# Optimization experiments

Hardware: AMD Instinct MI355X
Metric: run time of the kernel (lower is better)

The kernel has to match this reference:

```python
import jax, jax.numpy as jnp
import numpy as np

PADDING = 2
STRIDE = 1

def setup_inputs() -> dict:
    key = jax.random.key(0)
    k1, k2 = jax.random.split(key)
    X = jax.random.normal(k1, (32, 32, 128, 128), dtype=jnp.float32)  # NCHW
    K = jax.random.normal(k2, (64, 32, 5, 5), dtype=jnp.float32)     # OIHW
    return {"X": X, "K": K}

def reference(X, K):
    # Faithful to the naive loop: zero-pad by PADDING on H and W, then a
    # stride-STRIDE cross-correlation (slice * kernel).sum() per output pixel
    # and output channel -> exactly a standard conv2d with no bias.
    out = jax.lax.conv_general_dilated(
        X, K,
        window_strides=(STRIDE, STRIDE),
        padding=[(PADDING, PADDING), (PADDING, PADDING)],
        dimension_numbers=("NCHW", "OIHW", "NCHW"),
    )
    return out
```

## Files before the change

### kernel.cpp

```cpp
#include <hip/hip_runtime.h>


#define C_IN 32
#define H 128
#define W 128
#define O_CH 64
#define KS 5
#define PAD 2
#define XH 20
#define XW 20
#define NSHIFT 25
#define KSLICE_US 4096
#define KP_BYTES (NSHIFT * KSLICE_US * 2)
#define SX_PLANE 12800

typedef __bf16 bf16x8 __attribute__((ext_vector_type(8)));
typedef float f32x4 __attribute__((ext_vector_type(4)));

static __device__ __forceinline__ unsigned short f2bf(float f) {
    unsigned int u = __float_as_uint(f);
    u += 0x7fffu + ((u >> 16) & 1u);
    return (unsigned short)(u >> 16);
}
static __device__ __forceinline__ float bf2f(unsigned short s) {
    return __uint_as_float(((unsigned int)s) << 16);
}
static __device__ __forceinline__ uint4 pack8(const unsigned short* v) {
    uint4 w;
    w.x = (unsigned)v[0] | ((unsigned)v[1] << 16);
    w.y = (unsigned)v[2] | ((unsigned)v[3] << 16);
    w.z = (unsigned)v[4] | ((unsigned)v[5] << 16);
    w.w = (unsigned)v[6] | ((unsigned)v[7] << 16);
    return w;
}

__global__ __launch_bounds__(256)
void pack_k_kernel(const float* __restrict__ K, unsigned short* __restrict__ Kp) {
    int t = blockIdx.x * 256 + threadIdx.x;
    int lp = t & 15;
    int u  = t >> 4;
    int g  = u & 3;  u >>= 2;
    int nf = u & 3;  u >>= 2;
    int hl = u & 1;  u >>= 1;
    int s  = u;
    int oc = nf * 16 + lp;
    unsigned short v[8];
#pragma unroll
    for (int j = 0; j < 8; ++j) {
        float f = K[(size_t)(oc * C_IN + g * 8 + j) * (KS * KS) + s];
        unsigned short hi = f2bf(f);
        v[j] = hl ? f2bf(f - bf2f(hi)) : hi;
    }
    ((uint4*)Kp)[t] = pack8(v);
}

template<bool USE_KP>
__global__ __launch_bounds__(256, 2)
void conv5x5_mfma2(const float* __restrict__ X, const float* __restrict__ K,
                   const unsigned short* __restrict__ Kp, float* __restrict__ out) {
    __shared__ __align__(16) unsigned short sX[2 * SX_PLANE];
    __shared__ __align__(16) unsigned short sK[2][KSLICE_US];

    const int tid  = threadIdx.x;
    const int lane = tid & 63;
    const int wv   = tid >> 6;
    const int lg   = lane >> 4;
    const int lp   = lane & 15;

    const int bid  = blockIdx.x;
    const int n    = bid >> 6;
    const int tile = bid & 63;
    const int ty0  = (tile >> 3) * 16;
    const int tx0  = (tile & 7) * 16;

    uint4 kq0, kq1;
    if (USE_KP) {
        const uint4* src = (const uint4*)Kp;
        kq0 = src[tid];
        kq1 = src[tid + 256];
    }

    const float* Xn = X + (size_t)n * C_IN * H * W;
    for (int i = tid; i < XH * 4 * XW; i += 256) {
        int x = i % XW;
        int t = i / XW;
        int g = t & 3;
        int y = t >> 2;
        int gx = tx0 + x - PAD;
        int gy = ty0 + y - PAD;
        bool inb = ((unsigned)gx < (unsigned)W) && ((unsigned)gy < (unsigned)H);
        const float* p = Xn + (size_t)(g * 8) * (H * W) + gy * W + gx;
        unsigned short hi8[8], lo8[8];
#pragma unroll
        for (int j = 0; j < 8; ++j) {
            float v = inb ? p[j * (H * W)] : 0.f;
            hi8[j] = f2bf(v);
            lo8[j] = f2bf(v - bf2f(hi8[j]));
        }
        ((uint4*)sX)[i] = pack8(hi8);
        ((uint4*)sX)[i + 1600] = pack8(lo8);
    }

    unsigned short kh[8], kl[8];
    const int f_nf = tid >> 6, f_g = (tid >> 4) & 3, f_lp = tid & 15;
    if (!USE_KP) {
#pragma unroll
        for (int j = 0; j < 8; ++j) {
            float f = K[(size_t)((f_nf * 16 + f_lp) * C_IN + f_g * 8 + j) * (KS * KS) + 0];
            kh[j] = f2bf(f);
            kl[j] = f2bf(f - bf2f(kh[j]));
        }
    }

    {
        uint4* dst = (uint4*)&sK[0][0];
        if (USE_KP) {
            dst[tid] = kq0;
            dst[tid + 256] = kq1;
        } else {
            int base = ((f_nf * 4 + f_g) * 16 + f_lp) * 8;
            *(uint4*)&sK[0][base] = *(uint4*)kh;
            *(uint4*)&sK[0][base + 2048] = *(uint4*)kl;
        }
    }
    __syncthreads();

    f32x4 acc[4][4];
#pragma unroll
    for (int mf = 0; mf < 4; ++mf)
#pragma unroll
        for (int nf = 0; nf < 4; ++nf)
            acc[mf][nf] = (f32x4){0.f, 0.f, 0.f, 0.f};

    int ky = 0, kx = 0;
#pragma unroll 1
    for (int s = 0; s < NSHIFT; ++s) {
        const int buf = s & 1;

        if (USE_KP) {
            if (s < NSHIFT - 1) {
                const uint4* src = (const uint4*)(Kp + (size_t)(s + 1) * KSLICE_US);
                kq0 = src[tid];
                kq1 = src[tid + 256];
            }
        } else {
            if (s < NSHIFT - 1) {
#pragma unroll
                for (int j = 0; j < 8; ++j) {
                    float f = K[(size_t)((f_nf * 16 + f_lp) * C_IN + f_g * 8 + j) * (KS * KS) + s + 1];
                    kh[j] = f2bf(f);
                    kl[j] = f2bf(f - bf2f(kh[j]));
                }
            }
        }

        bf16x8 bh[4], bl[4];
#pragma unroll
        for (int nf = 0; nf < 4; ++nf) {
            int off = ((nf * 4 + lg) * 16 + lp) * 8;
            bh[nf] = *(const bf16x8*)&sK[buf][off];
            bl[nf] = *(const bf16x8*)&sK[buf][off + 2048];
        }

        bf16x8 ah[4], al[4];
#pragma unroll
        for (int mf = 0; mf < 4; ++mf) {
            int off = (((wv * 4 + mf + ky) * 4 + lg) * XW + kx + lp) * 8;
            ah[mf] = *(const bf16x8*)&sX[off];
            al[mf] = *(const bf16x8*)&sX[off + SX_PLANE];
        }

#pragma unroll
        for (int mf = 0; mf < 4; ++mf)
#pragma unroll
            for (int nf = 0; nf < 4; ++nf)
                acc[mf][nf] = __builtin_amdgcn_mfma_f32_16x16x32_bf16(ah[mf], bh[nf], acc[mf][nf], 0, 0, 0);
#pragma unroll
        for (int mf = 0; mf < 4; ++mf)
#pragma unroll
            for (int nf = 0; nf < 4; ++nf)
                acc[mf][nf] = __builtin_amdgcn_mfma_f32_16x16x32_bf16(ah[mf], bl[nf], acc[mf][nf], 0, 0, 0);
#pragma unroll
        for (int mf = 0; mf < 4; ++mf)
#pragma unroll
            for (int nf = 0; nf < 4; ++nf)
                acc[mf][nf] = __builtin_amdgcn_mfma_f32_16x16x32_bf16(al[mf], bh[nf], acc[mf][nf], 0, 0, 0);

        if (s < NSHIFT - 1) {
            uint4* dst = (uint4*)&sK[buf ^ 1][0];
            if (USE_KP) {
                dst[tid] = kq0;
                dst[tid + 256] = kq1;
            } else {
                int base = ((f_nf * 4 + f_g) * 16 + f_lp) * 8;
                *(uint4*)&sK[buf ^ 1][base] = *(uint4*)kh;
                *(uint4*)&sK[buf ^ 1][base + 2048] = *(uint4*)kl;
            }
        }
        __syncthreads();

        if (++kx == KS) { kx = 0; ++ky; }
    }

#pragma unroll
    for (int mf = 0; mf < 4; ++mf) {
        int y = ty0 + wv * 4 + mf;
#pragma unroll
        for (int nf = 0; nf < 4; ++nf) {
            int oc = nf * 16 + lp;
            size_t idx = (((size_t)n * O_CH + oc) * H + y) * W + tx0 + lg * 4;
            *(float4*)&out[idx] = *(float4*)&acc[mf][nf];
        }
    }
}

extern "C" void kernel_launch(void* const* d_in, const int* in_sizes, int n_in,
                              void* d_out, int out_size, void* d_ws, size_t ws_size,
                              hipStream_t stream) {
    const float* X = (const float*)d_in[0];
    const float* K = (const float*)d_in[1];
    float* out = (float*)d_out;

    if (ws_size >= (size_t)KP_BYTES) {
        unsigned short* Kp = (unsigned short*)d_ws;
        pack_k_kernel<<<dim3(50), dim3(256), 0, stream>>>(K, Kp);
        conv5x5_mfma2<true><<<dim3(2048), dim3(256), 0, stream>>>(X, K, Kp, out);
    } else {
        conv5x5_mfma2<false><<<dim3(2048), dim3(256), 0, stream>>>(X, K, nullptr, out);
    }
}
```

Measured before the change: 283.1 us.

## Load weight fragments directly into registers and drop per-shift LDS barriers

Removes the shared-memory double buffer for the packed weight slices. Each lane now loads its MFMA B fragments straight from global memory into registers, with a two-deep register prefetch across pairs of shifts. This removes the 25 per-shift __syncthreads and the LDS write/read traffic for weights. In exchange every wave issues redundant global loads of the same slice, and the extra B-fragment registers raise register pressure at two blocks per CU.

After: 275.0 us. 2.9% less time.

```diff
diff --git a/kernel.cpp b/kernel.cpp
--- a/kernel.cpp
+++ b/kernel.cpp
@@ -54,18 +54,76 @@
     ((uint4*)Kp)[t] = pack8(v);
 }
 
+struct Bfrag { uint4 h[4]; uint4 l[4]; };
+
+template<bool USE_KP>
+static __device__ __forceinline__ void load_b(const uint4* kp4, const float* K,
+                                              int s, int lg, int lp, int lane_off,
+                                              Bfrag& b) {
+    if (USE_KP) {
+#pragma unroll
+        for (int nf = 0; nf < 4; ++nf) {
+            b.h[nf] = kp4[s * 512 + nf * 64 + lane_off];
+            b.l[nf] = kp4[s * 512 + 256 + nf * 64 + lane_off];
+        }
+    } else {
+#pragma unroll
+        for (int nf = 0; nf < 4; ++nf) {
+            unsigned short hi[8], lo[8];
+#pragma unroll
+            for (int j = 0; j < 8; ++j) {
+                float f = K[(size_t)((nf * 16 + lp) * C_IN + lg * 8 + j) * (KS * KS) + s];
+                hi[j] = f2bf(f);
+                lo[j] = f2bf(f - bf2f(hi[j]));
+            }
+            b.h[nf] = pack8(hi);
+            b.l[nf] = pack8(lo);
+        }
+    }
+}
+
+static __device__ __forceinline__ void do_shift(const unsigned short* sX, int s,
+                                                int wv, int lg, int lp,
+                                                const Bfrag& b, f32x4 acc[4][4]) {
+    const int ky = s / KS, kx = s % KS;
+    bf16x8 ah[4], al[4];
+#pragma unroll
+    for (int mf = 0; mf < 4; ++mf) {
+        int off = (((wv * 4 + mf + ky) * 4 + lg) * XW + kx + lp) * 8;
+        ah[mf] = *(const bf16x8*)&sX[off];
+        al[mf] = *(const bf16x8*)&sX[off + SX_PLANE];
+    }
+    const bf16x8* bh = (const bf16x8*)b.h;
+    const bf16x8* bl = (const bf16x8*)b.l;
+#pragma unroll
+    for (int mf = 0; mf < 4; ++mf)
+#pragma unroll
+        for (int nf = 0; nf < 4; ++nf)
+            acc[mf][nf] = __builtin_amdgcn_mfma_f32_16x16x32_bf16(ah[mf], bh[nf], acc[mf][nf], 0, 0, 0);
+#pragma unroll
+    for (int mf = 0; mf < 4; ++mf)
+#pragma unroll
+        for (int nf = 0; nf < 4; ++nf)
+            acc[mf][nf] = __builtin_amdgcn_mfma_f32_16x16x32_bf16(ah[mf], bl[nf], acc[mf][nf], 0, 0, 0);
+#pragma unroll
+    for (int mf = 0; mf < 4; ++mf)
+#pragma unroll
+        for (int nf = 0; nf < 4; ++nf)
+            acc[mf][nf] = __builtin_amdgcn_mfma_f32_16x16x32_bf16(al[mf], bh[nf], acc[mf][nf], 0, 0, 0);
+}
+
 template<bool USE_KP>
 __global__ __launch_bounds__(256, 2)
-void conv5x5_mfma2(const float* __restrict__ X, const float* __restrict__ K,
+void conv5x5_mfma3(const float* __restrict__ X, const float* __restrict__ K,
                    const unsigned short* __restrict__ Kp, float* __restrict__ out) {
     __shared__ __align__(16) unsigned short sX[2 * SX_PLANE];
-    __shared__ __align__(16) unsigned short sK[2][KSLICE_US];
 
     const int tid  = threadIdx.x;
     const int lane = tid & 63;
     const int wv   = tid >> 6;
     const int lg   = lane >> 4;
     const int lp   = lane & 15;
+    const int lane_off = lg * 16 + lp;
 
     const int bid  = blockIdx.x;
     const int n    = bid >> 6;
@@ -73,12 +131,7 @@
     const int ty0  = (tile >> 3) * 16;
     const int tx0  = (tile & 7) * 16;
 
-    uint4 kq0, kq1;
-    if (USE_KP) {
-        const uint4* src = (const uint4*)Kp;
-        kq0 = src[tid];
-        kq1 = src[tid + 256];
-    }
+    const uint4* kp4 = (const uint4*)Kp;
 
     const float* Xn = X + (size_t)n * C_IN * H * W;
     for (int i = tid; i < XH * 4 * XW; i += 256) {
@@ -101,106 +154,26 @@
         ((uint4*)sX)[i + 1600] = pack8(lo8);
     }
 
-    unsigned short kh[8], kl[8];
-    const int f_nf = tid >> 6, f_g = (tid >> 4) & 3, f_lp = tid & 15;
-    if (!USE_KP) {
-#pragma unroll
-        for (int j = 0; j < 8; ++j) {
-            float f = K[(size_t)((f_nf * 16 + f_lp) * C_IN + f_g * 8 + j) * (KS * KS) + 0];
-            kh[j] = f2bf(f);
-            kl[j] = f2bf(f - bf2f(kh[j]));
-        }
-    }
-
-    {
-        uint4* dst = (uint4*)&sK[0][0];
-        if (USE_KP) {
-            dst[tid] = kq0;
-            dst[tid + 256] = kq1;
-        } else {
-            int base = ((f_nf * 4 + f_g) * 16 + f_lp) * 8;
-            *(uint4*)&sK[0][base] = *(uint4*)kh;
-            *(uint4*)&sK[0][base + 2048] = *(uint4*)kl;
-        }
-    }
+    f32x4 acc[4][4];
+#pragma unroll
+    for (int mf = 0; mf < 4; ++mf)
+#pragma unroll
+        for (int nf = 0; nf < 4; ++nf)
+            acc[mf][nf] = (f32x4){0.f, 0.f, 0.f, 0.f};
+
+    Bfrag b0, b1;
+    load_b<USE_KP>(kp4, K, 0, lg, lp, lane_off, b0);
+
     __syncthreads();
 
-    f32x4 acc[4][4];
-#pragma unroll
-    for (int mf = 0; mf < 4; ++mf)
-#pragma unroll
-        for (int nf = 0; nf < 4; ++nf)
-            acc[mf][nf] = (f32x4){0.f, 0.f, 0.f, 0.f};
-
-    int ky = 0, kx = 0;
 #pragma unroll 1
-    for (int s = 0; s < NSHIFT; ++s) {
-        const int buf = s & 1;
-
-        if (USE_KP) {
-            if (s < NSHIFT - 1) {
-                const uint4* src = (const uint4*)(Kp + (size_t)(s + 1) * KSLICE_US);
-                kq0 = src[tid];
-                kq1 = src[tid + 256];
-            }
-        } else {
-            if (s < NSHIFT - 1) {
-#pragma unroll
-                for (int j = 0; j < 8; ++j) {
-                    float f = K[(size_t)((f_nf * 16 + f_lp) * C_IN + f_g * 8 + j) * (KS * KS) + s + 1];
-                    kh[j] = f2bf(f);
-                    kl[j] = f2bf(f - bf2f(kh[j]));
-                }
-            }
-        }
-
-        bf16x8 bh[4], bl[4];
-#pragma unroll
-        for (int nf = 0; nf < 4; ++nf) {
-            int off = ((nf * 4 + lg) * 16 + lp) * 8;
-            bh[nf] = *(const bf16x8*)&sK[buf][off];
-            bl[nf] = *(const bf16x8*)&sK[buf][off + 2048];
-        }
-
-        bf16x8 ah[4], al[4];
-#pragma unroll
-        for (int mf = 0; mf < 4; ++mf) {
-            int off = (((wv * 4 + mf + ky) * 4 + lg) * XW + kx + lp) * 8;
-            ah[mf] = *(const bf16x8*)&sX[off];
-            al[mf] = *(const bf16x8*)&sX[off + SX_PLANE];
-        }
-
-#pragma unroll
-        for (int mf = 0; mf < 4; ++mf)
-#pragma unroll
-            for (int nf = 0; nf < 4; ++nf)
-                acc[mf][nf] = __builtin_amdgcn_mfma_f32_16x16x32_bf16(ah[mf], bh[nf], acc[mf][nf], 0, 0, 0);
-#pragma unroll
-        for (int mf = 0; mf < 4; ++mf)
-#pragma unroll
-            for (int nf = 0; nf < 4; ++nf)
-                acc[mf][nf] = __builtin_amdgcn_mfma_f32_16x16x32_bf16(ah[mf], bl[nf], acc[mf][nf], 0, 0, 0);
-#pragma unroll
-        for (int mf = 0; mf < 4; ++mf)
-#pragma unroll
-            for (int nf = 0; nf < 4; ++nf)
-                acc[mf][nf] = __builtin_amdgcn_mfma_f32_16x16x32_bf16(al[mf], bh[nf], acc[mf][nf], 0, 0, 0);
-
-        if (s < NSHIFT - 1) {
-            uint4* dst = (uint4*)&sK[buf ^ 1][0];
-            if (USE_KP) {
-                dst[tid] = kq0;
-                dst[tid + 256] = kq1;
-            } else {
-                int base = ((f_nf * 4 + f_g) * 16 + f_lp) * 8;
-                *(uint4*)&sK[buf ^ 1][base] = *(uint4*)kh;
-                *(uint4*)&sK[buf ^ 1][base + 2048] = *(uint4*)kl;
-            }
-        }
-        __syncthreads();
-
-        if (++kx == KS) { kx = 0; ++ky; }
-    }
+    for (int s = 0; s < NSHIFT - 1; s += 2) {
+        load_b<USE_KP>(kp4, K, s + 1, lg, lp, lane_off, b1);
+        do_shift(sX, s, wv, lg, lp, b0, acc);
+        load_b<USE_KP>(kp4, K, (s + 2 <= NSHIFT - 1) ? s + 2 : NSHIFT - 1, lg, lp, lane_off, b0);
+        do_shift(sX, s + 1, wv, lg, lp, b1, acc);
+    }
+    do_shift(sX, NSHIFT - 1, wv, lg, lp, b0, acc);
 
 #pragma unroll
     for (int mf = 0; mf < 4; ++mf) {
@@ -224,8 +197,8 @@
     if (ws_size >= (size_t)KP_BYTES) {
         unsigned short* Kp = (unsigned short*)d_ws;
         pack_k_kernel<<<dim3(50), dim3(256), 0, stream>>>(K, Kp);
-        conv5x5_mfma2<true><<<dim3(2048), dim3(256), 0, stream>>>(X, K, Kp, out);
+        conv5x5_mfma3<true><<<dim3(2048), dim3(256), 0, stream>>>(X, K, Kp, out);
     } else {
-        conv5x5_mfma2<false><<<dim3(2048), dim3(256), 0, stream>>>(X, K, nullptr, out);
-    }
-}
+        conv5x5_mfma3<false><<<dim3(2048), dim3(256), 0, stream>>>(X, K, nullptr, out);
+    }
+}
```
